# Performance work log

Hardware: AMD Instinct MI355X
Metric: run time of the kernel (lower is better)

The kernel has to match this reference:

```python
import jax, jax.numpy as jnp
import numpy as np

BATCH, LEN, D_MODEL, D_STATE = 2, 512, 256, 64


def setup_inputs() -> dict:
    key = jax.random.key(0)
    k = jax.random.split(key, 5)
    x = jax.random.normal(k[0], (BATCH, LEN, D_MODEL), jnp.float32)
    # A scaled by 1/d_state so the 512-step recurrence stays numerically finite
    # (raw randn A explodes under (I + dt*A)^L; the math is unchanged).
    A = jax.random.normal(k[1], (D_STATE, D_STATE), jnp.float32) / D_STATE
    B = jax.random.normal(k[2], (D_STATE, 1), jnp.float32)
    C = jax.random.normal(k[3], (D_MODEL, D_STATE), jnp.float32)
    D = jax.random.normal(k[4], (D_MODEL, 1), jnp.float32)
    log_dt = jnp.array([np.log(0.01)], jnp.float32)  # dt in [dt_min, dt_max]
    return {"x": x, "A": A, "B": B, "C": C, "D": D, "log_dt": log_dt}


def _ssm(u, A, Bvec, C, Dvec, dt):
    # u: (B, L, Dm). Torch: u_t = u[:, t, :, None] (B, Dm, 1)
    #   h <- h + dt * (h @ A.T + u_t @ B.T)   h: (B, Dm, N)
    #   y_t = h @ C.T + u_t @ D.T             y_t: (B, Dm, d_model)
    uB = u[..., None] * Bvec                  # (B, L, Dm, N) == u_t @ B.T
    uB_t = jnp.moveaxis(uB, 1, 0)             # (L, B, Dm, N) for scan
    h0 = jnp.zeros((u.shape[0], u.shape[2], A.shape[0]), u.dtype)

    def step(h, ub):
        h = h + dt * (h @ A.T + ub)
        return h, h

    _, hs = jax.lax.scan(step, h0, uB_t)      # hs: (L, B, Dm, N)
    # y = h @ C.T  (contract state dim) + u_t @ D.T (outer product)
    y = jnp.einsum('lbdn,mn->bldm', hs, C) + u[..., None] * Dvec
    return y                                   # (B, L, Dm, d_model)


def reference(x, A, B, C, D, log_dt):
    dt = jnp.exp(log_dt)[0]
    Bvec, Dvec = B[:, 0], D[:, 0]
    out = _ssm(x, A, Bvec, C, Dvec, dt)
    # bidirectional: run on time-reversed input, flip result back, add
    out_bwd = _ssm(x[:, ::-1], A, Bvec, C, Dvec, dt)
    return out + out_bwd[:, ::-1]
```

## Files before the change

kernel.cpp:

```cpp
#include <hip/hip_runtime.h>

#define P_TERMS 24

typedef _Float16 f16x8 __attribute__((ext_vector_type(8)));
typedef float f32x16 __attribute__((ext_vector_type(16)));

static __device__ __forceinline__ unsigned pk2(float a, float b) {
  unsigned d;
  asm("v_cvt_pkrtz_f16_f32 %0, %1, %2" : "=v"(d) : "v"(a), "v"(b));
  return d;
}
static __device__ __forceinline__ unsigned pkadd_sw(unsigned a, unsigned b) {
  unsigned d;
  asm("v_pk_add_f16 %0, %1, %2 op_sel:[0,1] op_sel_hi:[1,0]"
      : "=v"(d) : "v"(a), "v"(b));
  return d;
}

__global__ __launch_bounds__(256) void s4_powers(
    const float* __restrict__ A, const float* __restrict__ B,
    float* __restrict__ Fp) {
  __shared__ float cp[P_TERMS + 1][64];
  __shared__ float cur[64];
  const int tid = threadIdx.x;
  if (tid < 64) { cur[tid] = B[tid]; cp[0][tid] = B[tid]; }
  __syncthreads();
  const int n = tid >> 2, g = tid & 3;
  for (int p = 1; p <= P_TERMS; ++p) {
    float s = 0.f;
    const int j0 = g * 16;
#pragma unroll
    for (int j = 0; j < 16; ++j) s += A[n * 64 + j0 + j] * cur[j0 + j];
    s += __shfl_xor(s, 1);
    s += __shfl_xor(s, 2);
    __syncthreads();
    if (g == 0) { cur[n] = s; cp[p][n] = s; }
    __syncthreads();
  }
  for (int i = tid; i < (P_TERMS + 1) * 64; i += 256)
    Fp[i] = cp[i >> 6][i & 63];
}

__global__ __launch_bounds__(512) void s4_h8(
    const float* __restrict__ Fp, const float* __restrict__ log_dt,
    _Float16* __restrict__ H8) {
  __shared__ float Fm[P_TERMS + 1];
  const int n = blockIdx.x;
  const int k = threadIdx.x;
  if (k <= P_TERMS) Fm[k] = Fp[k * 64 + n];
  __syncthreads();
  const float dt = __expf(log_dt[0]);
  float coef = 1.f, s = Fm[0];
#pragma unroll 1
  for (int p = 1; p <= P_TERMS; ++p) {
    coef *= dt * (float)(k - p + 1) / (float)p;
    s += coef * Fm[p];
  }
  H8[((size_t)(k >> 3) * 64 + n) * 8 + (k & 7)] = (_Float16)s;
}

__global__ __launch_bounds__(256) void s4_ct(
    const float* __restrict__ C, _Float16* __restrict__ Ct8) {
  const int n = blockIdx.x;
  const int m = threadIdx.x;
  Ct8[((size_t)(n >> 3) * 256 + m) * 8 + (n & 7)] = (_Float16)C[m * 64 + n];
}

__global__ __launch_bounds__(256, 2) void s4_main(
    const float* __restrict__ x, const _Float16* __restrict__ H8,
    const _Float16* __restrict__ Ct8, const float* __restrict__ Dvec,
    const float* __restrict__ log_dt, float* __restrict__ out) {
  __shared__ float us[512];
  __shared__ uint4 UF8[1536];
  __shared__ unsigned Zl[256][34];

  const int tid = threadIdx.x;
  const int bid = blockIdx.x;
  const int th = bid & 1;
  const int ch = bid >> 1;
  const int b = ch >> 8;
  const int d = ch & 255;

  for (int i = tid; i < 512; i += 256) us[i] = x[(b * 512 + i) * 256 + d];
  __syncthreads();
  {
    const int i0 = tid * 6;
    float w[14];
#pragma unroll
    for (int j = 0; j < 14; ++j) {
      const int g = i0 + j - 512;
      const float v = us[g & 511];
      w[j] = (g >= 0 && g < 512) ? v : 0.f;
    }
    unsigned P[13];
#pragma unroll
    for (int j = 0; j < 13; ++j) P[j] = pk2(w[j], w[j + 1]);
#pragma unroll
    for (int e = 0; e < 6; ++e)
      UF8[i0 + e] = make_uint4(P[e], P[e + 2], P[e + 4], P[e + 6]);
  }
  __syncthreads();

  const int lane = tid & 63;
  const int wid = tid >> 6;
  const int r = lane & 31;
  const int hi = lane >> 5;
  const int tw = wid * 64;
  const int tg0 = th * 256 + tw;
  const int tl0 = tw + r;

  f32x16 acc[2][2];
#pragma unroll
  for (int ti = 0; ti < 2; ++ti)
#pragma unroll
    for (int ni = 0; ni < 2; ++ni)
#pragma unroll
      for (int e = 0; e < 16; ++e) acc[ti][ni][e] = 0.f;

  int ifj = 512 + tg0 + r + hi * 8;
  int irj = 505 + tg0 + r - hi * 8;
  const _Float16* hp = H8 + hi * 512 + r * 8;

#pragma unroll 1
  for (int j = 0; j < 32; ++j) {
    const uint4 F0 = UF8[ifj];
    const uint4 R0 = UF8[irj];
    const uint4 F1 = UF8[ifj + 32];
    const uint4 R1 = UF8[irj + 32];
    const f16x8 h0 = *reinterpret_cast<const f16x8*>(hp);
    const f16x8 h1 = *reinterpret_cast<const f16x8*>(hp + 256);
    union { unsigned w[4]; f16x8 v; } g0, g1;
    g0.w[0] = pkadd_sw(F0.x, R0.w);
    g0.w[1] = pkadd_sw(F0.y, R0.z);
    g0.w[2] = pkadd_sw(F0.z, R0.y);
    g0.w[3] = pkadd_sw(F0.w, R0.x);
    g1.w[0] = pkadd_sw(F1.x, R1.w);
    g1.w[1] = pkadd_sw(F1.y, R1.z);
    g1.w[2] = pkadd_sw(F1.z, R1.y);
    g1.w[3] = pkadd_sw(F1.w, R1.x);
    __builtin_amdgcn_s_setprio(1);
    acc[0][0] = __builtin_amdgcn_mfma_f32_32x32x16_f16(h0, g0.v, acc[0][0], 0, 0, 0);
    acc[0][1] = __builtin_amdgcn_mfma_f32_32x32x16_f16(h1, g0.v, acc[0][1], 0, 0, 0);
    acc[1][0] = __builtin_amdgcn_mfma_f32_32x32x16_f16(h0, g1.v, acc[1][0], 0, 0, 0);
    acc[1][1] = __builtin_amdgcn_mfma_f32_32x32x16_f16(h1, g1.v, acc[1][1], 0, 0, 0);
    __builtin_amdgcn_s_setprio(0);
    ifj += 16;
    irj -= 16;
    hp += 1024;
  }

#pragma unroll
  for (int ti = 0; ti < 2; ++ti) {
    const int t = tl0 + ti * 32;
#pragma unroll
    for (int ni = 0; ni < 2; ++ni) {
#pragma unroll
      for (int q = 0; q < 4; ++q) {
        uint2 v;
        v.x = pk2(acc[ti][ni][4 * q + 0], acc[ti][ni][4 * q + 1]);
        v.y = pk2(acc[ti][ni][4 * q + 2], acc[ti][ni][4 * q + 3]);
        *reinterpret_cast<uint2*>(&Zl[t][ni * 16 + q * 4 + 2 * hi]) = v;
      }
    }
  }

  const float dtv = __expf(log_dt[0]);
#pragma unroll 1
  for (int mp = 0; mp < 4; ++mp) {
    const int mb2 = mp * 64;
    f32x16 y[2][2];
#pragma unroll
    for (int ti = 0; ti < 2; ++ti)
#pragma unroll
      for (int mi = 0; mi < 2; ++mi)
#pragma unroll
        for (int e = 0; e < 16; ++e) y[ti][mi][e] = 0.f;

#pragma unroll
    for (int ks = 0; ks < 4; ++ks) {
      const int c0 = 8 * ks + 4 * hi;
      union { uint2 u[2]; f16x8 v; } z0, z1;
      z0.u[0] = *reinterpret_cast<const uint2*>(&Zl[tl0][c0]);
      z0.u[1] = *reinterpret_cast<const uint2*>(&Zl[tl0][c0 + 2]);
      z1.u[0] = *reinterpret_cast<const uint2*>(&Zl[tl0 + 32][c0]);
      z1.u[1] = *reinterpret_cast<const uint2*>(&Zl[tl0 + 32][c0 + 2]);
      const _Float16* cb = Ct8 + ((size_t)(2 * ks + hi) * 256 + mb2 + r) * 8;
      const f16x8 c0f = *reinterpret_cast<const f16x8*>(cb);
      const f16x8 c1f = *reinterpret_cast<const f16x8*>(cb + 256);
      __builtin_amdgcn_s_setprio(1);
      y[0][0] = __builtin_amdgcn_mfma_f32_32x32x16_f16(z0.v, c0f, y[0][0], 0, 0, 0);
      y[0][1] = __builtin_amdgcn_mfma_f32_32x32x16_f16(z0.v, c1f, y[0][1], 0, 0, 0);
      y[1][0] = __builtin_amdgcn_mfma_f32_32x32x16_f16(z1.v, c0f, y[1][0], 0, 0, 0);
      y[1][1] = __builtin_amdgcn_mfma_f32_32x32x16_f16(z1.v, c1f, y[1][1], 0, 0, 0);
      __builtin_amdgcn_s_setprio(0);
    }

#pragma unroll
    for (int ti = 0; ti < 2; ++ti) {
      const int tb2 = th * 256 + tw + ti * 32 + 4 * hi;
#pragma unroll
      for (int mi = 0; mi < 2; ++mi) {
        const int m = mb2 + mi * 32 + r;
        const float Dm = Dvec[m];
#pragma unroll
        for (int reg = 0; reg < 16; ++reg) {
          const int trow = tb2 + (reg & 3) + 8 * (reg >> 2);
          const float uv = us[trow];
          out[(((size_t)b * 512 + trow) * 256 + d) * 256 + m] =
              dtv * y[ti][mi][reg] + 2.f * uv * Dm;
        }
      }
    }
  }
}

extern "C" void kernel_launch(void* const* d_in, const int* in_sizes, int n_in,
                              void* d_out, int out_size, void* d_ws, size_t ws_size,
                              hipStream_t stream) {
  (void)in_sizes; (void)n_in; (void)out_size; (void)ws_size;
  const float* x = (const float*)d_in[0];
  const float* A = (const float*)d_in[1];
  const float* B = (const float*)d_in[2];
  const float* C = (const float*)d_in[3];
  const float* D = (const float*)d_in[4];
  const float* log_dt = (const float*)d_in[5];
  float* out = (float*)d_out;

  float* Fp = (float*)d_ws;
  _Float16* H8 = (_Float16*)((char*)d_ws + 8192);
  _Float16* Ct8 = (_Float16*)((char*)d_ws + 73728);

  s4_powers<<<1, 256, 0, stream>>>(A, B, Fp);
  s4_h8<<<64, 512, 0, stream>>>(Fp, log_dt, H8);
  s4_ct<<<64, 256, 0, stream>>>(C, Ct8);
  s4_main<<<1024, 256, 0, stream>>>(x, H8, Ct8, D, log_dt, out);
}
```

Measured before the change: 86.05 us.

## Merge time-halves into one block and interleave stage-1 MFMA with stage-2 stores

Each block now handles both 256-step time halves of a channel instead of launching one block per half, halving the grid and the shared-memory input setup per half. The second half's state-projection MFMA loop is split into four chunks, each interleaved with an output panel of the first half, so matrix work can overlap the large global stores. This adds register pressure from a second accumulator set and makes each block run longer, which may leave the GPU with fewer blocks to balance across.

```diff
diff --git a/kernel.cpp b/kernel.cpp
--- a/kernel.cpp
+++ b/kernel.cpp
@@ -75,9 +75,7 @@
   __shared__ unsigned Zl[256][34];
 
   const int tid = threadIdx.x;
-  const int bid = blockIdx.x;
-  const int th = bid & 1;
-  const int ch = bid >> 1;
+  const int ch = blockIdx.x;
   const int b = ch >> 8;
   const int d = ch & 255;
 
@@ -106,23 +104,10 @@
   const int r = lane & 31;
   const int hi = lane >> 5;
   const int tw = wid * 64;
-  const int tg0 = th * 256 + tw;
   const int tl0 = tw + r;
-
-  f32x16 acc[2][2];
-#pragma unroll
-  for (int ti = 0; ti < 2; ++ti)
-#pragma unroll
-    for (int ni = 0; ni < 2; ++ni)
-#pragma unroll
-      for (int e = 0; e < 16; ++e) acc[ti][ni][e] = 0.f;
-
-  int ifj = 512 + tg0 + r + hi * 8;
-  int irj = 505 + tg0 + r - hi * 8;
-  const _Float16* hp = H8 + hi * 512 + r * 8;
-
-#pragma unroll 1
-  for (int j = 0; j < 32; ++j) {
+  const float dtv = __expf(log_dt[0]);
+
+  auto s1_step = [&](int& ifj, int& irj, const _Float16*& hp, f32x16 acc[2][2]) {
     const uint4 F0 = UF8[ifj];
     const uint4 R0 = UF8[irj];
     const uint4 F1 = UF8[ifj + 32];
@@ -147,26 +132,26 @@
     ifj += 16;
     irj -= 16;
     hp += 1024;
-  }
-
-#pragma unroll
-  for (int ti = 0; ti < 2; ++ti) {
-    const int t = tl0 + ti * 32;
-#pragma unroll
-    for (int ni = 0; ni < 2; ++ni) {
-#pragma unroll
-      for (int q = 0; q < 4; ++q) {
-        uint2 v;
-        v.x = pk2(acc[ti][ni][4 * q + 0], acc[ti][ni][4 * q + 1]);
-        v.y = pk2(acc[ti][ni][4 * q + 2], acc[ti][ni][4 * q + 3]);
-        *reinterpret_cast<uint2*>(&Zl[t][ni * 16 + q * 4 + 2 * hi]) = v;
+  };
+
+  auto writeZ = [&](f32x16 acc[2][2]) {
+#pragma unroll
+    for (int ti = 0; ti < 2; ++ti) {
+      const int t = tl0 + ti * 32;
+#pragma unroll
+      for (int ni = 0; ni < 2; ++ni) {
+#pragma unroll
+        for (int q = 0; q < 4; ++q) {
+          uint2 v;
+          v.x = pk2(acc[ti][ni][4 * q + 0], acc[ti][ni][4 * q + 1]);
+          v.y = pk2(acc[ti][ni][4 * q + 2], acc[ti][ni][4 * q + 3]);
+          *reinterpret_cast<uint2*>(&Zl[t][ni * 16 + q * 4 + 2 * hi]) = v;
+        }
       }
     }
-  }
-
-  const float dtv = __expf(log_dt[0]);
-#pragma unroll 1
-  for (int mp = 0; mp < 4; ++mp) {
+  };
+
+  auto s2_panel = [&](int mp, int th) {
     const int mb2 = mp * 64;
     f32x16 y[2][2];
 #pragma unroll
@@ -175,7 +160,6 @@
       for (int mi = 0; mi < 2; ++mi)
 #pragma unroll
         for (int e = 0; e < 16; ++e) y[ti][mi][e] = 0.f;
-
 #pragma unroll
     for (int ks = 0; ks < 4; ++ks) {
       const int c0 = 8 * ks + 4 * hi;
@@ -194,7 +178,6 @@
       y[1][1] = __builtin_amdgcn_mfma_f32_32x32x16_f16(z1.v, c1f, y[1][1], 0, 0, 0);
       __builtin_amdgcn_s_setprio(0);
     }
-
 #pragma unroll
     for (int ti = 0; ti < 2; ++ti) {
       const int tb2 = th * 256 + tw + ti * 32 + 4 * hi;
@@ -211,7 +194,48 @@
         }
       }
     }
-  }
+  };
+
+  f32x16 acc[2][2];
+#pragma unroll
+  for (int ti = 0; ti < 2; ++ti)
+#pragma unroll
+    for (int ni = 0; ni < 2; ++ni)
+#pragma unroll
+      for (int e = 0; e < 16; ++e) acc[ti][ni][e] = 0.f;
+
+  {
+    int ifj = 512 + tw + r + hi * 8;
+    int irj = 505 + tw + r - hi * 8;
+    const _Float16* hp = H8 + hi * 512 + r * 8;
+#pragma unroll 1
+    for (int j = 0; j < 32; ++j) s1_step(ifj, irj, hp, acc);
+  }
+  writeZ(acc);
+
+  {
+    int ifj = 512 + 256 + tw + r + hi * 8;
+    int irj = 505 + 256 + tw + r - hi * 8;
+    const _Float16* hp = H8 + hi * 512 + r * 8;
+    f32x16 acc1[2][2];
+#pragma unroll
+    for (int ti = 0; ti < 2; ++ti)
+#pragma unroll
+      for (int ni = 0; ni < 2; ++ni)
+#pragma unroll
+        for (int e = 0; e < 16; ++e) acc1[ti][ni][e] = 0.f;
+
+#pragma unroll 1
+    for (int s = 0; s < 4; ++s) {
+#pragma unroll 1
+      for (int j2 = 0; j2 < 8; ++j2) s1_step(ifj, irj, hp, acc1);
+      s2_panel(s, 0);
+    }
+    writeZ(acc1);
+  }
+
+#pragma unroll 1
+  for (int s = 0; s < 4; ++s) s2_panel(s, 1);
 }
 
 extern "C" void kernel_launch(void* const* d_in, const int* in_sizes, int n_in,
@@ -233,5 +257,5 @@
   s4_powers<<<1, 256, 0, stream>>>(A, B, Fp);
   s4_h8<<<64, 512, 0, stream>>>(Fp, log_dt, H8);
   s4_ct<<<64, 256, 0, stream>>>(C, Ct8);
-  s4_main<<<1024, 256, 0, stream>>>(x, H8, Ct8, D, log_dt, out);
-}
+  s4_main<<<512, 256, 0, stream>>>(x, H8, Ct8, D, log_dt, out);
+}
```

Result: no change. 85.13 us (-1.1%).

## Fuse prep kernels and keep second-GEMM operands in registers via permlane swap

Applied to the files above, without the earlier changes.

Merges the three setup kernels into one 65-block prep kernel. Each of 64 blocks redundantly computes the A-power series and then its own column of the H kernel, and one extra block transposes C. In the main kernel, the LDS round-trip that reshapes the first MFMA output into the second MFMA's A operand is replaced with v_permlane32_swap register shuffles, and launch bounds are raised to allow 4 blocks per CU. This removes two kernel launches, an LDS buffer and its barrier-free reads. In exchange the power computation is repeated 64 times and register pressure rises under the tighter occupancy bound.

```diff
diff --git a/kernel.cpp b/kernel.cpp
--- a/kernel.cpp
+++ b/kernel.cpp
@@ -17,12 +17,21 @@
   return d;
 }
 
-__global__ __launch_bounds__(256) void s4_powers(
+__global__ __launch_bounds__(256) void s4_prep(
     const float* __restrict__ A, const float* __restrict__ B,
-    float* __restrict__ Fp) {
+    const float* __restrict__ C, const float* __restrict__ log_dt,
+    _Float16* __restrict__ H8, _Float16* __restrict__ Ct8) {
+  const int tid = threadIdx.x;
+  const int bid = blockIdx.x;
+  if (bid == 64) {
+    const int m = tid;
+#pragma unroll 1
+    for (int n = 0; n < 64; ++n)
+      Ct8[((size_t)(n >> 3) * 256 + m) * 8 + (n & 7)] = (_Float16)C[m * 64 + n];
+    return;
+  }
   __shared__ float cp[P_TERMS + 1][64];
   __shared__ float cur[64];
-  const int tid = threadIdx.x;
   if (tid < 64) { cur[tid] = B[tid]; cp[0][tid] = B[tid]; }
   __syncthreads();
   const int n = tid >> 2, g = tid & 3;
@@ -37,42 +46,25 @@
     if (g == 0) { cur[n] = s; cp[p][n] = s; }
     __syncthreads();
   }
-  for (int i = tid; i < (P_TERMS + 1) * 64; i += 256)
-    Fp[i] = cp[i >> 6][i & 63];
-}
-
-__global__ __launch_bounds__(512) void s4_h8(
-    const float* __restrict__ Fp, const float* __restrict__ log_dt,
-    _Float16* __restrict__ H8) {
-  __shared__ float Fm[P_TERMS + 1];
-  const int n = blockIdx.x;
-  const int k = threadIdx.x;
-  if (k <= P_TERMS) Fm[k] = Fp[k * 64 + n];
-  __syncthreads();
   const float dt = __expf(log_dt[0]);
-  float coef = 1.f, s = Fm[0];
-#pragma unroll 1
-  for (int p = 1; p <= P_TERMS; ++p) {
-    coef *= dt * (float)(k - p + 1) / (float)p;
-    s += coef * Fm[p];
-  }
-  H8[((size_t)(k >> 3) * 64 + n) * 8 + (k & 7)] = (_Float16)s;
-}
-
-__global__ __launch_bounds__(256) void s4_ct(
-    const float* __restrict__ C, _Float16* __restrict__ Ct8) {
-  const int n = blockIdx.x;
-  const int m = threadIdx.x;
-  Ct8[((size_t)(n >> 3) * 256 + m) * 8 + (n & 7)] = (_Float16)C[m * 64 + n];
-}
-
-__global__ __launch_bounds__(256, 2) void s4_main(
+#pragma unroll 1
+  for (int kk = tid; kk < 512; kk += 256) {
+    float coef = 1.f, s = cp[0][bid];
+#pragma unroll 1
+    for (int p = 1; p <= P_TERMS; ++p) {
+      coef *= dt * (float)(kk - p + 1) / (float)p;
+      s += coef * cp[p][bid];
+    }
+    H8[((size_t)(kk >> 3) * 64 + bid) * 8 + (kk & 7)] = (_Float16)s;
+  }
+}
+
+__global__ __launch_bounds__(256, 4) void s4_main(
     const float* __restrict__ x, const _Float16* __restrict__ H8,
     const _Float16* __restrict__ Ct8, const float* __restrict__ Dvec,
     const float* __restrict__ log_dt, float* __restrict__ out) {
   __shared__ float us[512];
   __shared__ uint4 UF8[1536];
-  __shared__ unsigned Zl[256][34];
 
   const int tid = threadIdx.x;
   const int bid = blockIdx.x;
@@ -107,7 +99,6 @@
   const int hi = lane >> 5;
   const int tw = wid * 64;
   const int tg0 = th * 256 + tw;
-  const int tl0 = tw + r;
 
   f32x16 acc[2][2];
 #pragma unroll
@@ -149,18 +140,26 @@
     hp += 1024;
   }
 
+  f16x8 zfrag[2][4];
 #pragma unroll
   for (int ti = 0; ti < 2; ++ti) {
-    const int t = tl0 + ti * 32;
-#pragma unroll
-    for (int ni = 0; ni < 2; ++ni) {
-#pragma unroll
-      for (int q = 0; q < 4; ++q) {
-        uint2 v;
-        v.x = pk2(acc[ti][ni][4 * q + 0], acc[ti][ni][4 * q + 1]);
-        v.y = pk2(acc[ti][ni][4 * q + 2], acc[ti][ni][4 * q + 3]);
-        *reinterpret_cast<uint2*>(&Zl[t][ni * 16 + q * 4 + 2 * hi]) = v;
-      }
+#pragma unroll
+    for (int ks = 0; ks < 4; ++ks) {
+      const int ni = ks >> 1;
+      const int qe = (2 * ks) & 3;
+      const int qo = qe + 1;
+      unsigned W0 = pk2(acc[ti][ni][4 * qe + 0], acc[ti][ni][4 * qe + 1]);
+      unsigned W2 = pk2(acc[ti][ni][4 * qo + 0], acc[ti][ni][4 * qo + 1]);
+      unsigned W1 = pk2(acc[ti][ni][4 * qe + 2], acc[ti][ni][4 * qe + 3]);
+      unsigned W3 = pk2(acc[ti][ni][4 * qo + 2], acc[ti][ni][4 * qo + 3]);
+      asm("v_permlane32_swap_b32 %0, %1" : "+v"(W0), "+v"(W2));
+      asm("v_permlane32_swap_b32 %0, %1" : "+v"(W1), "+v"(W3));
+      union { unsigned w[4]; f16x8 v; } zf;
+      zf.w[0] = W0;
+      zf.w[1] = W1;
+      zf.w[2] = W2;
+      zf.w[3] = W3;
+      zfrag[ti][ks] = zf.v;
     }
   }
 
@@ -178,20 +177,14 @@
 
 #pragma unroll
     for (int ks = 0; ks < 4; ++ks) {
-      const int c0 = 8 * ks + 4 * hi;
-      union { uint2 u[2]; f16x8 v; } z0, z1;
-      z0.u[0] = *reinterpret_cast<const uint2*>(&Zl[tl0][c0]);
-      z0.u[1] = *reinterpret_cast<const uint2*>(&Zl[tl0][c0 + 2]);
-      z1.u[0] = *reinterpret_cast<const uint2*>(&Zl[tl0 + 32][c0]);
-      z1.u[1] = *reinterpret_cast<const uint2*>(&Zl[tl0 + 32][c0 + 2]);
       const _Float16* cb = Ct8 + ((size_t)(2 * ks + hi) * 256 + mb2 + r) * 8;
       const f16x8 c0f = *reinterpret_cast<const f16x8*>(cb);
       const f16x8 c1f = *reinterpret_cast<const f16x8*>(cb + 256);
       __builtin_amdgcn_s_setprio(1);
-      y[0][0] = __builtin_amdgcn_mfma_f32_32x32x16_f16(z0.v, c0f, y[0][0], 0, 0, 0);
-      y[0][1] = __builtin_amdgcn_mfma_f32_32x32x16_f16(z0.v, c1f, y[0][1], 0, 0, 0);
-      y[1][0] = __builtin_amdgcn_mfma_f32_32x32x16_f16(z1.v, c0f, y[1][0], 0, 0, 0);
-      y[1][1] = __builtin_amdgcn_mfma_f32_32x32x16_f16(z1.v, c1f, y[1][1], 0, 0, 0);
+      y[0][0] = __builtin_amdgcn_mfma_f32_32x32x16_f16(zfrag[0][ks], c0f, y[0][0], 0, 0, 0);
+      y[0][1] = __builtin_amdgcn_mfma_f32_32x32x16_f16(zfrag[0][ks], c1f, y[0][1], 0, 0, 0);
+      y[1][0] = __builtin_amdgcn_mfma_f32_32x32x16_f16(zfrag[1][ks], c0f, y[1][0], 0, 0, 0);
+      y[1][1] = __builtin_amdgcn_mfma_f32_32x32x16_f16(zfrag[1][ks], c1f, y[1][1], 0, 0, 0);
       __builtin_amdgcn_s_setprio(0);
     }
 
@@ -226,12 +219,9 @@
   const float* log_dt = (const float*)d_in[5];
   float* out = (float*)d_out;
 
-  float* Fp = (float*)d_ws;
-  _Float16* H8 = (_Float16*)((char*)d_ws + 8192);
-  _Float16* Ct8 = (_Float16*)((char*)d_ws + 73728);
-
-  s4_powers<<<1, 256, 0, stream>>>(A, B, Fp);
-  s4_h8<<<64, 512, 0, stream>>>(Fp, log_dt, H8);
-  s4_ct<<<64, 256, 0, stream>>>(C, Ct8);
+  _Float16* H8 = (_Float16*)d_ws;
+  _Float16* Ct8 = (_Float16*)((char*)d_ws + 65536);
+
+  s4_prep<<<65, 256, 0, stream>>>(A, B, C, log_dt, H8, Ct8);
   s4_main<<<1024, 256, 0, stream>>>(x, H8, Ct8, D, log_dt, out);
 }
```

Result: slower. 93.91 us (+9.1%).
